# Kernel optimization log

Hardware: AMD Instinct MI355X
Metric: run time of the kernel (lower is better)

## Reference

```python
import jax, jax.numpy as jnp
import numpy as np

B, T, C_IN, C_OUT, H = 64, 512, 64, 64, 512


def setup_inputs() -> dict:
    key = jax.random.key(0)
    ks = jax.random.split(key, 24)
    s = 1.0 / np.sqrt(H)

    def p(k, shape):
        return (jax.random.uniform(k, shape, jnp.float32) * 2.0 - 1.0) * s

    inp = {
        "x": jax.random.normal(ks[0], (B, C_IN, T), jnp.float32),
        "frame_0": jax.random.normal(ks[1], (B, C_OUT, 1), jnp.float32),
    }
    i = 2
    for pre, in0 in (("enc", C_IN), ("dec", C_OUT)):
        for l, ins in enumerate((in0, H)):
            inp[f"{pre}_Wih{l}"] = p(ks[i], (3 * H, ins)); i += 1
            inp[f"{pre}_Whh{l}"] = p(ks[i], (3 * H, H)); i += 1
            inp[f"{pre}_bih{l}"] = p(ks[i], (3 * H,)); i += 1
            inp[f"{pre}_bhh{l}"] = p(ks[i], (3 * H,)); i += 1
    inp["fc_W"] = p(ks[i], (C_OUT, H)); i += 1
    inp["fc_b"] = p(ks[i], (C_OUT,))
    return inp


def _gru_cell(h, x, Wih, Whh, bih, bhh):
    # PyTorch GRU cell math: r,z,n gate ordering
    gi = x @ Wih.T + bih            # [B, 3H]
    gh = h @ Whh.T + bhh            # [B, 3H]
    ir, iz, inn = jnp.split(gi, 3, axis=-1)
    hr, hz, hn = jnp.split(gh, 3, axis=-1)
    r = jax.nn.sigmoid(ir + hr)
    z = jax.nn.sigmoid(iz + hz)
    n = jnp.tanh(inn + r * hn)
    return (1.0 - z) * n + z * h


def reference(x, frame_0,
              enc_Wih0, enc_Whh0, enc_bih0, enc_bhh0,
              enc_Wih1, enc_Whh1, enc_bih1, enc_bhh1,
              dec_Wih0, dec_Whh0, dec_bih0, dec_bhh0,
              dec_Wih1, dec_Whh1, dec_bih1, dec_bhh1,
              fc_W, fc_b):
    Bq = x.shape[0]
    num_steps = x.shape[-1]
    seq = jnp.transpose(x, (2, 0, 1))          # [T, B, C_in]
    f0 = frame_0[:, :, 0]                       # [B, C_out]

    enc_params = [(enc_Wih0, enc_Whh0, enc_bih0, enc_bhh0),
                  (enc_Wih1, enc_Whh1, enc_bih1, enc_bhh1)]
    dec_params = [(dec_Wih0, dec_Whh0, dec_bih0, dec_bhh0),
                  (dec_Wih1, dec_Whh1, dec_bih1, dec_bhh1)]

    # --- encoder: stacked GRU over T, zero initial hidden ---
    hiddens = []
    for (Wih, Whh, bih, bhh) in enc_params:
        h0 = jnp.zeros((Bq, Whh.shape[1]), seq.dtype)

        def step(h, xt, Wih=Wih, Whh=Whh, bih=bih, bhh=bhh):
            hn = _gru_cell(h, xt, Wih, Whh, bih, bhh)
            return hn, hn

        hT, seq = jax.lax.scan(step, h0, seq)   # seq becomes layer output [T,B,H]
        hiddens.append(hT)

    (W0, U0, b0, c0), (W1, U1, b1, c1) = dec_params

    def dec_step(carry, _):
        h0, h1, frame = carry
        h0n = _gru_cell(h0, frame, W0, U0, b0, c0)
        h1n = _gru_cell(h1, h0n, W1, U1, b1, c1)
        out = h1n @ fc_W.T + fc_b               # [B, C_out]
        return (h0n, h1n, out), out

    _, outs = jax.lax.scan(dec_step, (hiddens[0], hiddens[1], f0), None, length=num_steps)
    # outs: [T, B, C_out] -> (B, C_out, T)
    return jnp.transpose(outs, (1, 2, 0))
```

## Files before the change

kernel.cpp:

```cpp
#include <hip/hip_runtime.h>

#define H     512
#define BQ    64
#define TT    512
#define CIN   64
#define COUT  64
#define NWG   132
#define THREADS 256
#define RSLOTS 32

typedef unsigned int  uint;
typedef unsigned short ushort;
typedef unsigned long long u64;
typedef short bf16x8 __attribute__((ext_vector_type(8)));
typedef float f32x4  __attribute__((ext_vector_type(4)));

#define GH_BASE   0
#define GI_BASE   65536
#define GI0_BASE  131072
#define STG_BASE  139264
#define SMEM_SIZE 141312

#define WS_FLAGS  0
#define WS_BAR_SZ 16384
#define WS_BP     16384
#define WS_F0H    22528
#define WS_F0L    30720
#define WS_H0RH   65536
#define WS_H0RL   2162688
#define WS_H1RH   4259840
#define WS_H1RL   6356992
#define WS_M      8454144

#define SLOT(s)   (((s) & (RSLOTS-1)) * 32768)

struct Params {
  const float *x, *f0;
  const float *eWih0,*eWhh0,*ebih0,*ebhh0,*eWih1,*eWhh1,*ebih1,*ebhh1;
  const float *dWih0,*dWhh0,*dbih0,*dbhh0,*dWih1,*dWhh1,*dbih1,*dbhh1;
  const float *fcW,*fcb;
  float* out;
  char* ws;
};

__device__ __forceinline__ ushort f2bf(float v){
  uint b = __float_as_uint(v);
  return (ushort)((b + 0x7FFFu + ((b >> 16) & 1u)) >> 16);
}
__device__ __forceinline__ float bf2f(ushort u){ return __uint_as_float(((uint)u) << 16); }

__device__ __forceinline__ void gbar(uint* flags, uint r, int wg, int tid, bool rel, bool inv){
  __syncthreads();
  if (tid == 0){
    if (rel) __builtin_amdgcn_fence(__ATOMIC_RELEASE, "agent");
    __hip_atomic_store(&flags[wg*16], r, __ATOMIC_RELAXED, __HIP_MEMORY_SCOPE_AGENT);
  }
  asm volatile("" ::: "memory");
  if (tid < NWG){
    uint it = 0;
    while (__hip_atomic_load(&flags[tid*16], __ATOMIC_RELAXED, __HIP_MEMORY_SCOPE_AGENT) < r){
      __builtin_amdgcn_s_sleep(1);
      if ((++it & 1023u) == 0u) __builtin_amdgcn_fence(__ATOMIC_ACQUIRE, "agent");
    }
  }
  __syncthreads();
  if (inv) __builtin_amdgcn_fence(__ATOMIC_ACQUIRE, "agent");
}

template<int K>
__device__ void packW(char* lds, int base, const float* __restrict__ W, int colbase, int tid){
  for (int e = tid; e < 32*K; e += THREADS){
    int S = e / K, k = e - S*K;
    int gate = S & 3, hcl = S >> 2;
    float v = (gate < 3) ? W[(gate*H + colbase + hcl)*K + k] : 0.f;
    ushort hi = f2bf(v);
    ushort lo = f2bf(v - bf2f(hi));
    int tau = S >> 4, s = S & 15;
    int off = ((s*K + k)*2) ^ ((s & 7) << 4);
    char* tb = lds + base + tau*(16*K*4);
    *(ushort*)(tb + off) = hi;
    *(ushort*)(tb + 16*K*2 + off) = lo;
  }
}

__device__ void packFC(char* lds, const float* __restrict__ fcW, int colbase, int tid){
  for (int e = tid; e < 16*512; e += THREADS){
    int s = e >> 9, k = e & 511;
    float v = fcW[(colbase + s)*512 + k];
    ushort hi = f2bf(v);
    ushort lo = f2bf(v - bf2f(hi));
    int off = ((s*512 + k)*2) ^ ((s & 7) << 4);
    *(ushort*)(lds + off) = hi;
    *(ushort*)(lds + 16*512*2 + off) = lo;
  }
}

__device__ __forceinline__ void loadBias(const float* __restrict__ src, int colbase, int c, float* b){
#pragma unroll
  for (int tau = 0; tau < 2; ++tau){
    int gate = c & 3, hcl = 4*tau + (c >> 2);
    b[tau] = (gate < 3) ? src[gate*H + colbase + hcl] : 0.f;
  }
}

__device__ __forceinline__ void loadHold(const ushort* rh, const ushort* rl, int colb,
                                         int m, int lane, f32x4* hold){
  int c = lane & 15, g = lane >> 4;
#pragma unroll
  for (int tau = 0; tau < 2; ++tau){
    int col = colb + 4*tau + (c >> 2);
#pragma unroll
    for (int q = 0; q < 4; ++q){
      int row = m*16 + g*4 + q;
      int off = (col >> 3)*512 + row*8 + (col & 7);
      hold[tau][q] = bf2f(rh[off]) + bf2f(rl[off]);
    }
  }
}

template<int NTAU, int K, bool BLK>
__device__ __forceinline__ void gemm(const ushort* __restrict__ AH, const ushort* __restrict__ AL,
                                     const char* lds, int base, const float* bias,
                                     int m, int lane, f32x4* pre){
  const int c = lane & 15, g = lane >> 4;
  const int row = m*16 + c;
  constexpr int NK = K/32;
  bf16x8 ahv[NK], alv[NK];
#pragma unroll
  for (int kc = 0; kc < NK; ++kc){
    const int aoff = BLK ? ((kc*4 + g)*512 + row*8) : (row*K + kc*32 + g*8);
    ahv[kc] = *(const bf16x8*)(AH + aoff);
    alv[kc] = *(const bf16x8*)(AL + aoff);
  }
  f32x4 a1[NTAU], a2[NTAU];
#pragma unroll
  for (int tau = 0; tau < NTAU; ++tau){
    a1[tau] = f32x4{bias[tau], bias[tau], bias[tau], bias[tau]};
    a2[tau] = f32x4{0.f, 0.f, 0.f, 0.f};
  }
#pragma unroll
  for (int kc = 0; kc < NK; ++kc){
    const int off = ((c*K + kc*32 + g*8)*2) ^ ((c & 7) << 4);
#pragma unroll
    for (int tau = 0; tau < NTAU; ++tau){
      const char* tb = lds + base + tau*(16*K*4);
      bf16x8 wh = *(const bf16x8*)(tb + off);
      bf16x8 wl = *(const bf16x8*)(tb + 16*K*2 + off);
      a1[tau] = __builtin_amdgcn_mfma_f32_16x16x32_bf16(ahv[kc], wh, a1[tau], 0, 0, 0);
      a2[tau] = __builtin_amdgcn_mfma_f32_16x16x32_bf16(ahv[kc], wl, a2[tau], 0, 0, 0);
      a2[tau] = __builtin_amdgcn_mfma_f32_16x16x32_bf16(alv[kc], wh, a2[tau], 0, 0, 0);
    }
  }
#pragma unroll
  for (int tau = 0; tau < NTAU; ++tau) pre[tau] = a1[tau] + a2[tau];
}

__device__ __forceinline__ void gates_stage(const f32x4* pgi, const f32x4* pgh, f32x4* hold,
                                            ushort* __restrict__ stH, ushort* __restrict__ stL,
                                            int m, int lane){
  const int c = lane & 15, g = lane >> 4;
#pragma unroll
  for (int tau = 0; tau < 2; ++tau){
    f32x4 s, n, hn, rsh, zsh;
#pragma unroll
    for (int q = 0; q < 4; ++q) s[q] = 1.f / (1.f + expf(-(pgi[tau][q] + pgh[tau][q])));
#pragma unroll
    for (int q = 0; q < 4; ++q) rsh[q] = __shfl_xor(s[q], 2, 64);
#pragma unroll
    for (int q = 0; q < 4; ++q) zsh[q] = __shfl_xor(s[q], 3, 64);
#pragma unroll
    for (int q = 0; q < 4; ++q) n[q] = tanhf(pgi[tau][q] + rsh[q]*pgh[tau][q]);
#pragma unroll
    for (int q = 0; q < 4; ++q) hn[q] = (1.f - zsh[q])*n[q] + zsh[q]*hold[tau][q];
    hold[tau] = hn;
    if ((c & 3) == 2){
      const int cl = 4*tau + (c >> 2);
#pragma unroll
      for (int q = 0; q < 4; ++q){
        const int row = m*16 + g*4 + q;
        ushort hi = f2bf(hn[q]);
        ushort lo = f2bf(hn[q] - bf2f(hi));
        stH[row*8 + cl] = hi;
        stL[row*8 + cl] = lo;
      }
    }
  }
}

__device__ __forceinline__ void ring_flush(ushort* __restrict__ dH, ushort* __restrict__ dL,
                                           const ushort* __restrict__ stH,
                                           const ushort* __restrict__ stL, int tid){
  if (tid < 128){
    u64 v = *(const u64*)(stH + tid*4);
    __hip_atomic_store((u64*)dH + tid, v, __ATOMIC_RELAXED, __HIP_MEMORY_SCOPE_AGENT);
  } else if (tid < 256){
    int t2 = tid - 128;
    u64 v = *(const u64*)(stL + t2*4);
    __hip_atomic_store((u64*)dL + t2, v, __ATOMIC_RELAXED, __HIP_MEMORY_SCOPE_AGENT);
  }
}

__device__ __forceinline__ f32x4 bc4(float v){ return f32x4{v, v, v, v}; }

__global__ __launch_bounds__(THREADS, 1) void rnn_persist(Params p){
  extern __shared__ char smem[];
  char* ws = p.ws;
  uint* flags = (uint*)(ws + WS_FLAGS);
  float*  bp   = (float*)(ws + WS_BP);
  ushort* f0H  = (ushort*)(ws + WS_F0H);
  ushort* f0L  = (ushort*)(ws + WS_F0L);
  ushort* h0rH = (ushort*)(ws + WS_H0RH);
  ushort* h0rL = (ushort*)(ws + WS_H0RL);
  ushort* h1rH = (ushort*)(ws + WS_H1RH);
  ushort* h1rL = (ushort*)(ws + WS_H1RL);
  float*  Mw   = (float*)(ws + WS_M);
  ushort* xTH  = (ushort*)(void*)p.out;
  ushort* xTL  = xTH + TT*BQ*CIN;
  ushort* stH  = (ushort*)(smem + STG_BASE);
  ushort* stL  = stH + 512;

  const int wg = blockIdx.x, tid = threadIdx.x;
  const int wid = tid >> 6, lane = tid & 63;
  const int c = lane & 15;
  const int gtid = wg*THREADS + tid;
  const int gstride = NWG*THREADS;
  uint bno = 0;

  for (int e = gtid; e < TT*BQ*CIN; e += gstride){
    int t = e >> 12, b = (e >> 6) & 63, cc = e & 63;
    float v = p.x[(b*CIN + cc)*TT + t];
    ushort hi = f2bf(v);
    xTH[e] = hi; xTL[e] = f2bf(v - bf2f(hi));
  }
  for (int e = gtid; e < BQ*COUT; e += gstride){
    float v = p.f0[e];
    ushort hi = f2bf(v);
    f0H[e] = hi; f0L[e] = f2bf(v - bf2f(hi));
  }
  {
    const int total = 1536*512;
    const int per = (total + gstride - 1) / gstride;
    const int start = gtid * per;
    for (int i = 0; i < per; ++i){
      int e = start + i;
      if (e >= total) break;
      int rr = e >> 9, q = e & 511;
      float acc = 0.f;
      for (int k = 0; k < 64; ++k) acc += p.dWih0[rr*64 + k] * p.fcW[k*512 + q];
      Mw[e] = acc;
    }
  }
  for (int e = gtid; e < 1536; e += gstride){
    float acc = p.dbih0[e];
    for (int k = 0; k < 64; ++k) acc += p.dWih0[e*64 + k] * p.fcb[k];
    bp[e] = acc;
  }
  gbar(flags, ++bno, wg, tid, true, true);

  const bool isA = (wg < 64), isB = (wg >= 64 && wg < 128);
  const int colb = isA ? wg*8 : (wg - 64)*8;
  const int kblk = colb >> 3;
  float bgi[2] = {0.f,0.f}, bgh[2] = {0.f,0.f}, bgi0[2] = {0.f,0.f}, bfc = 0.f;
  f32x4 hold[2]; hold[0] = bc4(0.f); hold[1] = bc4(0.f);
  int fccol = 0;
  if (isA){
    packW<64 >(smem, GI_BASE, p.eWih0, colb, tid);
    packW<512>(smem, GH_BASE, p.eWhh0, colb, tid);
    loadBias(p.ebih0, colb, c, bgi); loadBias(p.ebhh0, colb, c, bgh);
  } else if (isB){
    packW<512>(smem, GI_BASE, p.eWih1, colb, tid);
    packW<512>(smem, GH_BASE, p.eWhh1, colb, tid);
    loadBias(p.ebih1, colb, c, bgi); loadBias(p.ebhh1, colb, c, bgh);
  } else {
    fccol = (wg - 128)*16;
    packFC(smem, p.fcW, fccol, tid);
    bfc = p.fcb[fccol + c];
  }
  gbar(flags, ++bno, wg, tid, false, false);

  for (int r = 0; r <= TT; ++r){
    if (isA && r < TT){
      const int t = r;
      f32x4 pgi[2], pgh[2];
      if (t > 0)
        gemm<2,512,true>(h0rH + SLOT(t-1), h0rL + SLOT(t-1), smem, GH_BASE, bgh, wid, lane, pgh);
      else { pgh[0] = bc4(bgh[0]); pgh[1] = bc4(bgh[1]); }
      gemm<2,64,false>(xTH + t*4096, xTL + t*4096, smem, GI_BASE, bgi, wid, lane, pgi);
      gates_stage(pgi, pgh, hold, stH, stL, wid, lane);
      __syncthreads();
      ring_flush(h0rH + SLOT(t) + kblk*512, h0rL + SLOT(t) + kblk*512, stH, stL, tid);
    } else if (isB && r >= 1){
      const int t = r - 1;
      f32x4 pgi[2], pgh[2];
      if (t > 0)
        gemm<2,512,true>(h1rH + SLOT(t-1), h1rL + SLOT(t-1), smem, GH_BASE, bgh, wid, lane, pgh);
      else { pgh[0] = bc4(bgh[0]); pgh[1] = bc4(bgh[1]); }
      gemm<2,512,true>(h0rH + SLOT(t), h0rL + SLOT(t), smem, GI_BASE, bgi, wid, lane, pgi);
      gates_stage(pgi, pgh, hold, stH, stL, wid, lane);
      __syncthreads();
      ring_flush(h1rH + SLOT(t) + kblk*512, h1rL + SLOT(t) + kblk*512, stH, stL, tid);
    }
    ++bno;
    gbar(flags, bno, wg, tid, false, (bno & 15u) == 0u);
  }

  if (isA){
    packW<512>(smem, GH_BASE, p.dWhh0, colb, tid);
    packW<512>(smem, GI_BASE, Mw,      colb, tid);
    packW<64 >(smem, GI0_BASE, p.dWih0, colb, tid);
    loadBias(bp,      colb, c, bgi);
    loadBias(p.dbhh0, colb, c, bgh);
    loadBias(p.dbih0, colb, c, bgi0);
    loadHold(h0rH + SLOT(511), h0rL + SLOT(511), colb, wid, lane, hold);
  } else if (isB){
    packW<512>(smem, GI_BASE, p.dWih1, colb, tid);
    packW<512>(smem, GH_BASE, p.dWhh1, colb, tid);
    loadBias(p.dbih1, colb, c, bgi); loadBias(p.dbhh1, colb, c, bgh);
    loadHold(h1rH + SLOT(511), h1rL + SLOT(511), colb, wid, lane, hold);
  }
  gbar(flags, ++bno, wg, tid, false, true);

  f32x4 pgh_s[2]; pgh_s[0] = bc4(0.f); pgh_s[1] = bc4(0.f);
  for (int r = 0; r <= 2*TT; ++r){
    if (isA){
      if (r == 0){
        gemm<2,512,true>(h0rH + SLOT(511), h0rL + SLOT(511), smem, GH_BASE, bgh, wid, lane, pgh_s);
        f32x4 pgi[2];
        gemm<2,64,false>(f0H, f0L, smem, GI0_BASE, bgi0, wid, lane, pgi);
        gates_stage(pgi, pgh_s, hold, stH, stL, wid, lane);
        __syncthreads();
        ring_flush(h0rH + SLOT(512) + kblk*512, h0rL + SLOT(512) + kblk*512, stH, stL, tid);
      } else if (r & 1){
        const int t = (r + 1) >> 1;
        if (t < TT) gemm<2,512,true>(h0rH + SLOT(511+t), h0rL + SLOT(511+t), smem, GH_BASE, bgh, wid, lane, pgh_s);
      } else {
        const int t = r >> 1;
        if (t < TT){
          f32x4 pgi[2];
          gemm<2,512,true>(h1rH + SLOT(511+t), h1rL + SLOT(511+t), smem, GI_BASE, bgi, wid, lane, pgi);
          gates_stage(pgi, pgh_s, hold, stH, stL, wid, lane);
          __syncthreads();
          ring_flush(h0rH + SLOT(512+t) + kblk*512, h0rL + SLOT(512+t) + kblk*512, stH, stL, tid);
        }
      }
    } else if (isB){
      if (!(r & 1)){
        const int t = r >> 1;
        if (t < TT) gemm<2,512,true>(h1rH + SLOT(511+t), h1rL + SLOT(511+t), smem, GH_BASE, bgh, wid, lane, pgh_s);
      } else {
        const int t = r >> 1;
        f32x4 pgi[2];
        gemm<2,512,true>(h0rH + SLOT(512+t), h0rL + SLOT(512+t), smem, GI_BASE, bgi, wid, lane, pgi);
        gates_stage(pgi, pgh_s, hold, stH, stL, wid, lane);
        __syncthreads();
        ring_flush(h1rH + SLOT(512+t) + kblk*512, h1rL + SLOT(512+t) + kblk*512, stH, stL, tid);
      }
    } else {
      if (!(r & 1) && r >= 2){
        const int t = (r - 2) >> 1;
        f32x4 pre[1];
        gemm<1,512,true>(h1rH + SLOT(512+t), h1rL + SLOT(512+t), smem, 0, &bfc, wid, lane, pre);
        const int outcol = fccol + c, gq = lane >> 4;
#pragma unroll
        for (int q = 0; q < 4; ++q){
          const int row = wid*16 + gq*4 + q;
          p.out[(row*COUT + outcol)*TT + t] = pre[0][q];
        }
      }
    }
    ++bno;
    gbar(flags, bno, wg, tid, false, (bno & 15u) == 0u);
  }
}

extern "C" void kernel_launch(void* const* d_in, const int* in_sizes, int n_in,
                              void* d_out, int out_size, void* d_ws, size_t ws_size,
                              hipStream_t stream){
  Params p;
  p.x     = (const float*)d_in[0];  p.f0    = (const float*)d_in[1];
  p.eWih0 = (const float*)d_in[2];  p.eWhh0 = (const float*)d_in[3];
  p.ebih0 = (const float*)d_in[4];  p.ebhh0 = (const float*)d_in[5];
  p.eWih1 = (const float*)d_in[6];  p.eWhh1 = (const float*)d_in[7];
  p.ebih1 = (const float*)d_in[8];  p.ebhh1 = (const float*)d_in[9];
  p.dWih0 = (const float*)d_in[10]; p.dWhh0 = (const float*)d_in[11];
  p.dbih0 = (const float*)d_in[12]; p.dbhh0 = (const float*)d_in[13];
  p.dWih1 = (const float*)d_in[14]; p.dWhh1 = (const float*)d_in[15];
  p.dbih1 = (const float*)d_in[16]; p.dbhh1 = (const float*)d_in[17];
  p.fcW   = (const float*)d_in[18]; p.fcb   = (const float*)d_in[19];
  p.out = (float*)d_out;
  p.ws  = (char*)d_ws;

  hipFuncSetAttribute((const void*)rnn_persist, hipFuncAttributeMaxDynamicSharedMemorySize, SMEM_SIZE);
  hipMemsetAsync(d_ws, 0, WS_BAR_SZ, stream);
  hipLaunchKernelGGL(rnn_persist, dim3(NWG), dim3(THREADS), SMEM_SIZE, stream, p);
}
```

Before: 10.54 ms.

## Halve decoder grid barriers with targeted layer-0 ready flags

The decoder loop now takes one grid-wide barrier per time step instead of two. Layer-0 workgroups publish a per-workgroup progress flag after writing their hidden state. Layer-1 workgroups and the next layer-0 recurrent GEMM wait only on those 64 flags instead of a full barrier. This is meant to cut the cost of the decoder's serial barrier chain, at the price of extra flag traffic and more complex memory-ordering reasoning: the flag publish has no explicit release fence.

New measurement: 11.40 ms. 8.2% more time.

```diff
diff --git a/kernel.cpp b/kernel.cpp
--- a/kernel.cpp
+++ b/kernel.cpp
@@ -22,6 +22,7 @@
 #define SMEM_SIZE 141312
 
 #define WS_FLAGS  0
+#define WS_FA     8448
 #define WS_BAR_SZ 16384
 #define WS_BP     16384
 #define WS_F0H    22528
@@ -65,6 +66,20 @@
   }
   __syncthreads();
   if (inv) __builtin_amdgcn_fence(__ATOMIC_ACQUIRE, "agent");
+}
+
+__device__ __forceinline__ void waitS(const uint* __restrict__ f, uint thr, int tid){
+  if (tid < 64){
+    uint it = 0;
+    while (__hip_atomic_load(&f[tid*16], __ATOMIC_RELAXED, __HIP_MEMORY_SCOPE_AGENT) < thr){
+      __builtin_amdgcn_s_sleep(1);
+      if ((++it & 1023u) == 0u) __builtin_amdgcn_fence(__ATOMIC_ACQUIRE, "agent");
+    }
+  }
+  __syncthreads();
+}
+__device__ __forceinline__ void publish(uint* f, uint v){
+  __hip_atomic_store(f, v, __ATOMIC_RELAXED, __HIP_MEMORY_SCOPE_AGENT);
 }
 
 template<int K>
@@ -206,6 +221,7 @@
   extern __shared__ char smem[];
   char* ws = p.ws;
   uint* flags = (uint*)(ws + WS_FLAGS);
+  uint* fA    = (uint*)(ws + WS_FA);
   float*  bp   = (float*)(ws + WS_BP);
   ushort* f0H  = (ushort*)(ws + WS_F0H);
   ushort* f0L  = (ushort*)(ws + WS_F0L);
@@ -321,51 +337,44 @@
   gbar(flags, ++bno, wg, tid, false, true);
 
   f32x4 pgh_s[2]; pgh_s[0] = bc4(0.f); pgh_s[1] = bc4(0.f);
-  for (int r = 0; r <= 2*TT; ++r){
-    if (isA){
-      if (r == 0){
-        gemm<2,512,true>(h0rH + SLOT(511), h0rL + SLOT(511), smem, GH_BASE, bgh, wid, lane, pgh_s);
-        f32x4 pgi[2];
+  if (isA)
+    gemm<2,512,true>(h0rH + SLOT(511), h0rL + SLOT(511), smem, GH_BASE, bgh, wid, lane, pgh_s);
+
+  for (int t = 0; t <= TT; ++t){
+    if (isA && t < TT){
+      const int g = 512 + t;
+      f32x4 pgi[2];
+      if (t == 0)
         gemm<2,64,false>(f0H, f0L, smem, GI0_BASE, bgi0, wid, lane, pgi);
-        gates_stage(pgi, pgh_s, hold, stH, stL, wid, lane);
-        __syncthreads();
-        ring_flush(h0rH + SLOT(512) + kblk*512, h0rL + SLOT(512) + kblk*512, stH, stL, tid);
-      } else if (r & 1){
-        const int t = (r + 1) >> 1;
-        if (t < TT) gemm<2,512,true>(h0rH + SLOT(511+t), h0rL + SLOT(511+t), smem, GH_BASE, bgh, wid, lane, pgh_s);
-      } else {
-        const int t = r >> 1;
-        if (t < TT){
-          f32x4 pgi[2];
-          gemm<2,512,true>(h1rH + SLOT(511+t), h1rL + SLOT(511+t), smem, GI_BASE, bgi, wid, lane, pgi);
-          gates_stage(pgi, pgh_s, hold, stH, stL, wid, lane);
-          __syncthreads();
-          ring_flush(h0rH + SLOT(512+t) + kblk*512, h0rL + SLOT(512+t) + kblk*512, stH, stL, tid);
-        }
+      else
+        gemm<2,512,true>(h1rH + SLOT(g-1), h1rL + SLOT(g-1), smem, GI_BASE, bgi, wid, lane, pgi);
+      gates_stage(pgi, pgh_s, hold, stH, stL, wid, lane);
+      __syncthreads();
+      ring_flush(h0rH + SLOT(g) + kblk*512, h0rL + SLOT(g) + kblk*512, stH, stL, tid);
+      __syncthreads();
+      if (tid == 0) publish(&fA[wg*16], (uint)(t+1));
+      if (t < TT-1){
+        waitS(fA, (uint)(t+1), tid);
+        gemm<2,512,true>(h0rH + SLOT(g), h0rL + SLOT(g), smem, GH_BASE, bgh, wid, lane, pgh_s);
       }
-    } else if (isB){
-      if (!(r & 1)){
-        const int t = r >> 1;
-        if (t < TT) gemm<2,512,true>(h1rH + SLOT(511+t), h1rL + SLOT(511+t), smem, GH_BASE, bgh, wid, lane, pgh_s);
-      } else {
-        const int t = r >> 1;
-        f32x4 pgi[2];
-        gemm<2,512,true>(h0rH + SLOT(512+t), h0rL + SLOT(512+t), smem, GI_BASE, bgi, wid, lane, pgi);
-        gates_stage(pgi, pgh_s, hold, stH, stL, wid, lane);
-        __syncthreads();
-        ring_flush(h1rH + SLOT(512+t) + kblk*512, h1rL + SLOT(512+t) + kblk*512, stH, stL, tid);
-      }
-    } else {
-      if (!(r & 1) && r >= 2){
-        const int t = (r - 2) >> 1;
-        f32x4 pre[1];
-        gemm<1,512,true>(h1rH + SLOT(512+t), h1rL + SLOT(512+t), smem, 0, &bfc, wid, lane, pre);
-        const int outcol = fccol + c, gq = lane >> 4;
-#pragma unroll
-        for (int q = 0; q < 4; ++q){
-          const int row = wid*16 + gq*4 + q;
-          p.out[(row*COUT + outcol)*TT + t] = pre[0][q];
-        }
+    } else if (isB && t < TT){
+      const int g = 512 + t;
+      f32x4 pgh[2], pgi[2];
+      gemm<2,512,true>(h1rH + SLOT(g-1), h1rL + SLOT(g-1), smem, GH_BASE, bgh, wid, lane, pgh);
+      waitS(fA, (uint)(t+1), tid);
+      gemm<2,512,true>(h0rH + SLOT(g), h0rL + SLOT(g), smem, GI_BASE, bgi, wid, lane, pgi);
+      gates_stage(pgi, pgh, hold, stH, stL, wid, lane);
+      __syncthreads();
+      ring_flush(h1rH + SLOT(g) + kblk*512, h1rL + SLOT(g) + kblk*512, stH, stL, tid);
+    } else if (!isA && !isB && t >= 1){
+      const int g = 511 + t;
+      f32x4 pre[1];
+      gemm<1,512,true>(h1rH + SLOT(g), h1rL + SLOT(g), smem, 0, &bfc, wid, lane, pre);
+      const int outcol = fccol + c, gq = lane >> 4;
+#pragma unroll
+      for (int q = 0; q < 4; ++q){
+        const int row = wid*16 + gq*4 + q;
+        p.out[(row*COUT + outcol)*TT + (t-1)] = pre[0][q];
       }
     }
     ++bno;
```
